# Optimization experiments

Hardware: AMD Instinct MI355X
Metric: run time of the kernel (lower is better)

The kernel has to match this reference:

```python
import jax, jax.numpy as jnp
import numpy as np

NEG_INF = -1e9

def apply_rope(x, positions, head_dim, theta):
    # x: [B, S, H, Dh]; positions: [S] int32
    half = head_dim // 2
    fraction = (2.0 / head_dim) * jnp.arange(half, dtype=jnp.float32)  # [Dh/2]
    timescale = theta ** fraction
    angle = positions.astype(jnp.float32)[:, None] / timescale  # [S, Dh/2]
    sin = jnp.sin(angle)[None, :, None, :]  # [1,S,1,Dh/2]
    cos = jnp.cos(angle)[None, :, None, :]
    x1, x2 = jnp.split(x, 2, axis=-1)
    out = jnp.concatenate([x1 * cos - x2 * sin, x2 * cos + x1 * sin], axis=-1)
    return out.astype(x.dtype)

def setup_inputs() -> dict:
    key = jax.random.key(0)
    B, S, D = 2, 2048, 2048
    Q, N, H = 16, 4, 128
    ks = jax.random.split(key, 5)
    scale = 1.0 / np.sqrt(D)
    return {
        "x": jax.random.normal(ks[0], (B, S, D), dtype=jnp.float32),
        "positions": jnp.arange(S, dtype=jnp.int32),
        "Wq": jax.random.normal(ks[1], (Q, D, H), dtype=jnp.float32) * scale,
        "Wk": jax.random.normal(ks[2], (N, D, H), dtype=jnp.float32) * scale,
        "Wv": jax.random.normal(ks[3], (N, D, H), dtype=jnp.float32) * scale,
        "Wo": jax.random.normal(ks[4], (Q, H, D), dtype=jnp.float32) * scale,
    }

def reference(x, positions, Wq, Wk, Wv, Wo):
    head_dim = Wq.shape[-1]
    theta = 10000.0
    head_repeats = Wq.shape[0] // Wk.shape[0]  # GQA repeat factor

    q_BSQH = jnp.einsum('BSD,QDH->BSQH', x, Wq)
    q_BSQH = apply_rope(q_BSQH, positions, head_dim, theta)
    k_BTNH = jnp.einsum('BSD,NDH->BSNH', x, Wk)
    k_BTNH = apply_rope(k_BTNH, positions, head_dim, theta)
    v_BTNH = jnp.einsum('BSD,NDH->BSNH', x, Wv)

    k_BTQH = jnp.repeat(k_BTNH, head_repeats, axis=2)
    v_BTQH = jnp.repeat(v_BTNH, head_repeats, axis=2)

    scores_BQST = jnp.einsum('BSQH,BTQH->BQST', q_BSQH, k_BTQH) / jnp.sqrt(
        jnp.asarray(head_dim, dtype=x.dtype))
    S = q_BSQH.shape[1]
    causal = jnp.tril(jnp.ones((1, 1, S, S), dtype=jnp.bool_))
    scores_BQST = jnp.where(causal, scores_BQST, NEG_INF)
    weights_BQST = jax.nn.softmax(scores_BQST, axis=-1)
    out_BSQH = jnp.einsum('BQST,BTQH->BSQH', weights_BQST, v_BTQH)
    o_BSD = jnp.einsum('BSQH,QHD->BSD', out_BSQH, Wo)
    return o_BSD
```

## Files before the change

kernel.cpp:

```cpp
#include <hip/hip_runtime.h>
#include <math.h>

#define BB 2
#define SS 2048
#define DD 2048
#define QH 16
#define NKV 4
#define HD 128
#define REP 4
#define NEG_INF_F (-1e9f)

typedef __bf16 bfrag __attribute__((ext_vector_type(8)));
typedef float  ffrag __attribute__((ext_vector_type(4)));

__device__ inline unsigned short f2bf(float f) {
    unsigned u = __builtin_bit_cast(unsigned, f);
    u += 0x7fff + ((u >> 16) & 1);
    return (unsigned short)(u >> 16);
}
__device__ inline float bf2f(unsigned short u) {
    unsigned v = (unsigned)u << 16;
    return __builtin_bit_cast(float, v);
}
__device__ inline bfrag ld_frag(const unsigned short* p) {
    uint4 u = *(const uint4*)p;
    return __builtin_bit_cast(bfrag, u);
}
__device__ inline void async16(const void* g, void* l) {
    __builtin_amdgcn_global_load_lds(
        (const __attribute__((address_space(1))) unsigned int*)g,
        (__attribute__((address_space(3))) unsigned int*)l, 16, 0, 0);
}
__device__ inline unsigned pkbf(float a, float b) {
    unsigned short ua = __builtin_bit_cast(unsigned short, (__bf16)a);
    unsigned short ub = __builtin_bit_cast(unsigned short, (__bf16)b);
    return (unsigned)ua | ((unsigned)ub << 16);
}

__global__ void cast_x_kernel(const float* __restrict__ x,
                              unsigned short* __restrict__ xb, int n)
{
    const int i = (blockIdx.x * blockDim.x + threadIdx.x) * 8;
    if (i >= n) return;
    float4 a = *(const float4*)(x + i);
    float4 b = *(const float4*)(x + i + 4);
    unsigned short o[8];
    o[0] = f2bf(a.x); o[1] = f2bf(a.y); o[2] = f2bf(a.z); o[3] = f2bf(a.w);
    o[4] = f2bf(b.x); o[5] = f2bf(b.y); o[6] = f2bf(b.z); o[7] = f2bf(b.w);
    *(uint4*)(xb + i) = *(uint4*)o;
}

__global__ __launch_bounds__(256) void tcast_kernel(
    const float* __restrict__ in, unsigned short* __restrict__ out,
    int R, int C)
{
    __shared__ float tile[32][33];
    const size_t bofs = (size_t)blockIdx.z * R * C;
    in  += bofs;
    out += bofs;
    const int c0 = blockIdx.x * 32, r0 = blockIdx.y * 32;
    const int tx = threadIdx.x & 31, ty = threadIdx.x >> 5;
    #pragma unroll
    for (int k = 0; k < 4; ++k)
        tile[ty + 8 * k][tx] = in[(size_t)(r0 + ty + 8 * k) * C + c0 + tx];
    __syncthreads();
    #pragma unroll
    for (int k = 0; k < 4; ++k)
        out[(size_t)(c0 + ty + 8 * k) * R + r0 + tx] =
            f2bf(tile[tx][ty + 8 * k]);
}

__global__ __launch_bounds__(256) void gemm_bt_kernel(
    const unsigned short* __restrict__ A,
    const unsigned short* __restrict__ Bt,
    unsigned short* __restrict__ q_out, unsigned short* __restrict__ k_out,
    unsigned short* __restrict__ vt_out, float* __restrict__ f_out,
    int mode)
{
    const int gy = gridDim.y;
    int f = blockIdx.x * gy + blockIdx.y;
    const int chunk = (gridDim.x * gy) >> 3;
    f = (f & 7) * chunk + (f >> 3);
    const int m0 = (f / gy) * 128;
    const int n0 = (f % gy) * 128;

    const int tid  = threadIdx.x;
    const int w    = tid >> 6, lane = tid & 63;
    const int l16  = lane & 15, quad = lane >> 4;
    const int wm = (w >> 1) * 64, wn = (w & 1) * 64;
    const int sl4 = l16 & 3;

    __shared__ unsigned short As[2][128 * 32];
    __shared__ unsigned short Bs[2][128 * 32];

    ffrag acc[4][4];
    #pragma unroll
    for (int mi = 0; mi < 4; ++mi)
        #pragma unroll
        for (int ni = 0; ni < 4; ++ni)
            acc[mi][ni] = (ffrag){0.f, 0.f, 0.f, 0.f};

    auto stage = [&](int b, int k0) {
        #pragma unroll
        for (int j = 0; j < 2; ++j) {
            const int i   = (j * 4 + w) * 64 + lane;
            const int row = i >> 2;
            const int sl  = (i & 3) ^ (row & 3);
            async16(&A [(size_t)(m0 + row) * 2048 + k0 + sl * 8],
                    (char*)&As[b][0] + i * 16);
            async16(&Bt[(size_t)(n0 + row) * 2048 + k0 + sl * 8],
                    (char*)&Bs[b][0] + i * 16);
        }
    };

    stage(0, 0);
    __syncthreads();
    int cur = 0;
    for (int k0 = 0; k0 < 2048; k0 += 32) {
        if (k0 + 32 < 2048) stage(cur ^ 1, k0 + 32);

        bfrag af[4], bfr[4];
        #pragma unroll
        for (int mi = 0; mi < 4; ++mi)
            af[mi] = ld_frag(
                &As[cur][(wm + mi * 16 + l16) * 32 + (quad ^ sl4) * 8]);
        #pragma unroll
        for (int ni = 0; ni < 4; ++ni)
            bfr[ni] = ld_frag(
                &Bs[cur][(wn + ni * 16 + l16) * 32 + (quad ^ sl4) * 8]);
        #pragma unroll
        for (int mi = 0; mi < 4; ++mi)
            #pragma unroll
            for (int ni = 0; ni < 4; ++ni)
                acc[mi][ni] = __builtin_amdgcn_mfma_f32_16x16x32_bf16(
                    af[mi], bfr[ni], acc[mi][ni], 0, 0, 0);

        __syncthreads();
        cur ^= 1;
    }

    if (mode == 0) {
        #pragma unroll
        for (int mi = 0; mi < 4; ++mi)
            #pragma unroll
            for (int ni = 0; ni < 4; ++ni) {
                const int col = n0 + wn + ni * 16 + l16;
                #pragma unroll
                for (int r = 0; r < 4; ++r) {
                    const int row = m0 + wm + mi * 16 + quad * 4 + r;
                    f_out[(size_t)row * 2048 + col] = acc[mi][ni][r];
                }
            }
    } else if (n0 < 2560) {
        unsigned short* dst;
        int colbase, stride;
        if (n0 < 2048)      { dst = q_out; colbase = n0;        stride = 2048; }
        else                { dst = k_out; colbase = n0 - 2048; stride = 512;  }
        #pragma unroll
        for (int mi = 0; mi < 4; ++mi)
            #pragma unroll
            for (int ni = 0; ni < 4; ++ni) {
                const int col = colbase + wn + ni * 16 + l16;
                #pragma unroll
                for (int r = 0; r < 4; ++r) {
                    const int row = m0 + wm + mi * 16 + quad * 4 + r;
                    dst[(size_t)row * stride + col] = f2bf(acc[mi][ni][r]);
                }
            }
    } else {
        const int c3 = n0 - 2560;
        #pragma unroll
        for (int mi = 0; mi < 4; ++mi)
            #pragma unroll
            for (int ni = 0; ni < 4; ++ni) {
                const int col = c3 + wn + ni * 16 + l16;
                const int nh = col >> 7, h = col & 127;
                const int row0 = m0 + wm + mi * 16 + quad * 4;
                const int b = row0 >> 11, s = row0 & 2047;
                unsigned short pk[4];
                #pragma unroll
                for (int r = 0; r < 4; ++r) pk[r] = f2bf(acc[mi][ni][r]);
                *(uint2*)&vt_out[(((size_t)b * NKV + nh) * HD + h) * SS + s] =
                    *(uint2*)pk;
            }
    }
}

__global__ void rope_kernel(unsigned short* __restrict__ q,
                            unsigned short* __restrict__ k,
                            const int* __restrict__ positions)
{
    const int qpairs = BB * SS * QH * 64;
    const int kpairs = BB * SS * NKV * 64;
    int idx = blockIdx.x * blockDim.x + threadIdx.x;
    unsigned short* base;
    int nh;
    if (idx < qpairs) { base = q; nh = QH; }
    else {
        idx -= qpairs;
        if (idx >= kpairs) return;
        base = k; nh = NKV;
    }
    const int hh   = idx & 63;
    const int rest = idx >> 6;
    const int head = rest % nh;
    const int bs   = rest / nh;
    const int s    = bs % SS;

    unsigned short* p = base + ((size_t)bs * nh + head) * HD;
    const float pos = (float)positions[s];
    const float inv_ts = powf(10000.0f, -(float)hh * (1.0f / 64.0f));
    const float angle = pos * inv_ts;
    const float sn = sinf(angle), cs = cosf(angle);
    const float sc_ = (nh == QH) ? 0.08838834764831845f : 1.0f;
    const float x1 = bf2f(p[hh]), x2 = bf2f(p[hh + 64]);
    p[hh]      = f2bf((x1 * cs - x2 * sn) * sc_);
    p[hh + 64] = f2bf((x2 * cs + x1 * sn) * sc_);
}

__global__ __launch_bounds__(256, 2) void attn_kernel(
    const unsigned short* __restrict__ qb,
    const unsigned short* __restrict__ kb,
    const unsigned short* __restrict__ vt,
    unsigned short* __restrict__ o)
{
    int f = blockIdx.y * 16 + blockIdx.x;
    f = (f & 7) * 64 + (f >> 3);
    const int bh = f >> 4;
    const int bx = f & 15;

    const int b  = bh / QH, qh = bh % QH;
    const int n  = qh / REP;

    const int tid  = threadIdx.x;
    const int w    = tid >> 6;
    const int lane = tid & 63;
    const int l16  = lane & 15;
    const int quad = lane >> 4;
    const int sw   = l16 & 7;

    __shared__ unsigned short Ks[2][2][64][64];
    __shared__ unsigned short Vs[2][128][64];
    __shared__ unsigned short Ps[4][16][72];

    const unsigned short* kbase = kb + (size_t)b * (SS * NKV * HD) + n * HD;
    const unsigned short* vbase = vt + ((size_t)b * NKV + n) * HD * SS;

    for (int ph = 0; ph < 2; ++ph) {
        const int tile = ph == 0 ? (31 - bx) : bx;
        const int s0 = tile * 64;
        const int rbase = s0 + w * 16 + quad * 4;
        const int thr   = w * 16 + l16;

        bfrag qf[4];
        {
            const unsigned short* qp =
                qb + ((size_t)(b * SS + s0 + w * 16 + l16) * QH + qh) * HD
                   + quad * 8;
            #pragma unroll
            for (int c = 0; c < 4; ++c) qf[c] = ld_frag(qp + c * 32);
        }
        ffrag oacc[8];
        #pragma unroll
        for (int t = 0; t < 8; ++t) oacc[t] = (ffrag){0.f, 0.f, 0.f, 0.f};
        float mr = -1e30f, lr = 0.0f;

        #pragma unroll
        for (int j = 0; j < 4; ++j) {
            const int s = j * 256 + tid;
            {   const int cc = s >> 9, t = (s >> 3) & 63;
                const int sl = (s & 7) ^ (t & 7);
                async16(kbase + (size_t)t * (NKV * HD) + cc * 64 + sl * 8,
                        (char*)&Ks[0][0][0][0] + s * 16);
            }
            {   const int h = s >> 3, sl = (s & 7) ^ (h & 7);
                async16(vbase + (size_t)h * SS + sl * 8,
                        (char*)&Vs[0][0][0] + s * 16);
            }
        }
        __syncthreads();

        int p = 0;
        for (int t0 = 0; t0 <= s0; t0 += 64, p ^= 1) {
            if (t0 + 64 <= s0) {
                const int tn = t0 + 64;
                #pragma unroll
                for (int j = 0; j < 4; ++j) {
                    const int s = j * 256 + tid;
                    {   const int cc = s >> 9, t = (s >> 3) & 63;
                        const int sl = (s & 7) ^ (t & 7);
                        async16(kbase + (size_t)(tn + t) * (NKV * HD)
                                      + cc * 64 + sl * 8,
                                (char*)&Ks[p ^ 1][0][0][0] + s * 16);
                    }
                    {   const int h = s >> 3, sl = (s & 7) ^ (h & 7);
                        async16(vbase + (size_t)h * SS + tn + sl * 8,
                                (char*)&Vs[p ^ 1][0][0] + s * 16);
                    }
                }
            }

            ffrag sc[4];
            #pragma unroll
            for (int t = 0; t < 4; ++t) sc[t] = (ffrag){0.f, 0.f, 0.f, 0.f};
            __builtin_amdgcn_s_setprio(1);
            #pragma unroll
            for (int c = 0; c < 4; ++c) {
                const int cc = c >> 1, cb = (c & 1) * 4;
                #pragma unroll
                for (int t = 0; t < 4; ++t) {
                    bfrag kfr = ld_frag(
                        &Ks[p][cc][t * 16 + l16][((cb + quad) ^ sw) * 8]);
                    sc[t] = __builtin_amdgcn_mfma_f32_16x16x32_bf16(
                        kfr, qf[c], sc[t], 0, 0, 0);
                }
            }
            __builtin_amdgcn_s_setprio(0);

            const bool diag = (t0 == s0);
            if (diag) {
                #pragma unroll
                for (int t = 0; t < 4; ++t) {
                    const int col0 = t * 16 + quad * 4;
                    #pragma unroll
                    for (int r = 0; r < 4; ++r)
                        if (col0 + r > thr) sc[t][r] = NEG_INF_F;
                }
            }

            float tmax;
            {
                float a0 = fmaxf(fmaxf(sc[0][0], sc[0][1]),
                                 fmaxf(sc[0][2], sc[0][3]));
                float a1 = fmaxf(fmaxf(sc[1][0], sc[1][1]),
                                 fmaxf(sc[1][2], sc[1][3]));
                float a2 = fmaxf(fmaxf(sc[2][0], sc[2][1]),
                                 fmaxf(sc[2][2], sc[2][3]));
                float a3 = fmaxf(fmaxf(sc[3][0], sc[3][1]),
                                 fmaxf(sc[3][2], sc[3][3]));
                tmax = fmaxf(fmaxf(a0, a1), fmaxf(a2, a3));
            }
            tmax = fmaxf(tmax, __shfl_xor(tmax, 16));
            tmax = fmaxf(tmax, __shfl_xor(tmax, 32));

            if (__any(tmax > mr + 8.0f)) {
                const float mnew  = fmaxf(mr, tmax);
                const float alpha = __expf(mr - mnew);
                lr *= alpha;
                mr = mnew;
                #pragma unroll
                for (int r = 0; r < 4; ++r) {
                    const float ar =
                        __shfl(alpha, (lane & 48) | (quad * 4 + r));
                    #pragma unroll
                    for (int t = 0; t < 8; ++t) oacc[t][r] *= ar;
                }
            }

            float ps = 0.f;
            #pragma unroll
            for (int t = 0; t < 4; ++t) {
                const float p0 = __expf(sc[t][0] - mr);
                const float p1 = __expf(sc[t][1] - mr);
                const float p2 = __expf(sc[t][2] - mr);
                const float p3 = __expf(sc[t][3] - mr);
                ps += (p0 + p1) + (p2 + p3);
                uint2 pk2;
                pk2.x = pkbf(p0, p1);
                pk2.y = pkbf(p2, p3);
                *(uint2*)&Ps[w][l16][t * 16 + quad * 4] = pk2;
            }
            ps += __shfl_xor(ps, 16);
            ps += __shfl_xor(ps, 32);
            lr += ps;

            __builtin_amdgcn_s_setprio(1);
            #pragma unroll
            for (int c = 0; c < 2; ++c) {
                bfrag pf = ld_frag(&Ps[w][l16][c * 32 + quad * 8]);
                #pragma unroll
                for (int t = 0; t < 8; ++t) {
                    bfrag vf = ld_frag(
                        &Vs[p][t * 16 + l16][((c * 4 + quad) ^ sw) * 8]);
                    oacc[t] = __builtin_amdgcn_mfma_f32_16x16x32_bf16(
                        pf, vf, oacc[t], 0, 0, 0);
                }
            }
            __builtin_amdgcn_s_setprio(0);

            __syncthreads();
        }

        #pragma unroll
        for (int r = 0; r < 4; ++r) {
            const float lrr  = __shfl(lr, (lane & 48) | (quad * 4 + r));
            const float invl = 1.0f / lrr;
            const int row = rbase + r;
            unsigned short* op = o + ((size_t)(b * SS + row) * QH + qh) * HD;
            #pragma unroll
            for (int t = 0; t < 8; ++t)
                op[t * 16 + l16] = f2bf(oacc[t][r] * invl);
        }
    }
}

extern "C" void kernel_launch(void* const* d_in, const int* in_sizes, int n_in,
                              void* d_out, int out_size, void* d_ws,
                              size_t ws_size, hipStream_t stream)
{
    const float* x         = (const float*)d_in[0];
    const int*   positions = (const int*)d_in[1];
    const float* Wq        = (const float*)d_in[2];
    const float* Wk        = (const float*)d_in[3];
    const float* Wv        = (const float*)d_in[4];
    const float* Wo        = (const float*)d_in[5];
    float* out = (float*)d_out;

    char* ws = (char*)d_ws;
    unsigned short* xb    = (unsigned short*)ws;
    unsigned short* Wqkvt = (unsigned short*)(ws + (16u << 20));
    unsigned short* Wot   = (unsigned short*)(ws + (28u << 20));
    unsigned short* qbf   = (unsigned short*)(ws + (36u << 20));
    unsigned short* kbf   = (unsigned short*)(ws + (52u << 20));
    unsigned short* vtb   = (unsigned short*)(ws + (56u << 20));
    unsigned short* opre  = xb;

    const int nx = BB * SS * DD;
    cast_x_kernel<<<nx / (8 * 256), 256, 0, stream>>>(x, xb, nx);

    tcast_kernel<<<dim3(4, 64, 16), 256, 0, stream>>>(Wq, Wqkvt, 2048, 128);
    tcast_kernel<<<dim3(4, 64, 4), 256, 0, stream>>>(
        Wk, Wqkvt + (size_t)16 * 128 * 2048, 2048, 128);
    tcast_kernel<<<dim3(4, 64, 4), 256, 0, stream>>>(
        Wv, Wqkvt + (size_t)20 * 128 * 2048, 2048, 128);
    tcast_kernel<<<dim3(64, 64, 1), 256, 0, stream>>>(Wo, Wot, 2048, 2048);

    gemm_bt_kernel<<<dim3(32, 24), 256, 0, stream>>>(
        xb, Wqkvt, qbf, kbf, vtb, nullptr, 1);

    const int pairs = BB * SS * (QH + NKV) * 64;
    rope_kernel<<<(pairs + 255) / 256, 256, 0, stream>>>(qbf, kbf, positions);

    dim3 g2(16, BB * QH);
    attn_kernel<<<g2, 256, 0, stream>>>(qbf, kbf, vtb, opre);

    gemm_bt_kernel<<<dim3(32, 16), 256, 0, stream>>>(
        opre, Wot, nullptr, nullptr, nullptr, out, 0);
}
```

Baseline: 361.0 us.

## Replace 128x128 GEMM with 256x256 tile, 4-stage async pipeline and MFMA priority

Both projection GEMMs now use a new kernel with 256x256 output tiles, 512 threads and a 4-deep shared-memory ring of async loads. It uses explicit vmcnt waits and barriers, and raises wave priority around the MFMA bursts. The aim is more reuse of each loaded tile and better hiding of global-load latency. The trade-off is far fewer blocks: 192 for the QKV GEMM and 128 for the output GEMM on a 256-CU device, so many CUs may sit idle. The old XCD-aware block remapping is also dropped.

```diff
diff --git a/kernel.cpp b/kernel.cpp
--- a/kernel.cpp
+++ b/kernel.cpp
@@ -70,85 +70,98 @@
             f2bf(tile[tx][ty + 8 * k]);
 }
 
-__global__ __launch_bounds__(256) void gemm_bt_kernel(
+__global__ __launch_bounds__(512, 2) void gemm256_kernel(
     const unsigned short* __restrict__ A,
     const unsigned short* __restrict__ Bt,
     unsigned short* __restrict__ q_out, unsigned short* __restrict__ k_out,
     unsigned short* __restrict__ vt_out, float* __restrict__ f_out,
     int mode)
 {
-    const int gy = gridDim.y;
-    int f = blockIdx.x * gy + blockIdx.y;
-    const int chunk = (gridDim.x * gy) >> 3;
-    f = (f & 7) * chunk + (f >> 3);
-    const int m0 = (f / gy) * 128;
-    const int n0 = (f % gy) * 128;
-
+    const int m0 = blockIdx.x * 256;
+    const int n0 = blockIdx.y * 256;
     const int tid  = threadIdx.x;
-    const int w    = tid >> 6, lane = tid & 63;
+    const int wid  = tid >> 6, lane = tid & 63;
     const int l16  = lane & 15, quad = lane >> 4;
-    const int wm = (w >> 1) * 64, wn = (w & 1) * 64;
-    const int sl4 = l16 & 3;
-
-    __shared__ unsigned short As[2][128 * 32];
-    __shared__ unsigned short Bs[2][128 * 32];
-
-    ffrag acc[4][4];
+    const int wr   = wid >> 2, wc = wid & 3;
+    const int rs   = quad ^ (l16 & 3);
+
+    __shared__ unsigned short As[4][256 * 32];
+    __shared__ unsigned short Bs[4][256 * 32];
+
+    ffrag acc[8][4];
     #pragma unroll
-    for (int mi = 0; mi < 4; ++mi)
-        #pragma unroll
-        for (int ni = 0; ni < 4; ++ni)
-            acc[mi][ni] = (ffrag){0.f, 0.f, 0.f, 0.f};
-
-    auto stage = [&](int b, int k0) {
+    for (int mf = 0; mf < 8; ++mf)
+        #pragma unroll
+        for (int nf = 0; nf < 4; ++nf)
+            acc[mf][nf] = (ffrag){0.f, 0.f, 0.f, 0.f};
+
+    auto stage = [&](int d, int t) {
+        const int k0 = t * 32;
         #pragma unroll
         for (int j = 0; j < 2; ++j) {
-            const int i   = (j * 4 + w) * 64 + lane;
+            const int i   = j * 512 + tid;
             const int row = i >> 2;
             const int sl  = (i & 3) ^ (row & 3);
             async16(&A [(size_t)(m0 + row) * 2048 + k0 + sl * 8],
-                    (char*)&As[b][0] + i * 16);
+                    (char*)&As[d][0] + i * 16);
             async16(&Bt[(size_t)(n0 + row) * 2048 + k0 + sl * 8],
-                    (char*)&Bs[b][0] + i * 16);
+                    (char*)&Bs[d][0] + i * 16);
         }
     };
 
-    stage(0, 0);
-    __syncthreads();
-    int cur = 0;
-    for (int k0 = 0; k0 < 2048; k0 += 32) {
-        if (k0 + 32 < 2048) stage(cur ^ 1, k0 + 32);
-
-        bfrag af[4], bfr[4];
-        #pragma unroll
-        for (int mi = 0; mi < 4; ++mi)
-            af[mi] = ld_frag(
-                &As[cur][(wm + mi * 16 + l16) * 32 + (quad ^ sl4) * 8]);
-        #pragma unroll
-        for (int ni = 0; ni < 4; ++ni)
-            bfr[ni] = ld_frag(
-                &Bs[cur][(wn + ni * 16 + l16) * 32 + (quad ^ sl4) * 8]);
-        #pragma unroll
-        for (int mi = 0; mi < 4; ++mi)
-            #pragma unroll
-            for (int ni = 0; ni < 4; ++ni)
-                acc[mi][ni] = __builtin_amdgcn_mfma_f32_16x16x32_bf16(
-                    af[mi], bfr[ni], acc[mi][ni], 0, 0, 0);
-
-        __syncthreads();
-        cur ^= 1;
+    stage(0, 0); stage(1, 1); stage(2, 2);
+    asm volatile("s_waitcnt vmcnt(8)" ::: "memory");
+    __builtin_amdgcn_s_barrier();
+    __builtin_amdgcn_sched_barrier(0);
+
+    for (int T = 0; T < 64; ++T) {
+        if (T + 3 < 64) stage((T + 3) & 3, T + 3);
+
+        const int d = T & 3;
+        const unsigned short* ab = &As[d][0];
+        const unsigned short* bb = &Bs[d][0];
+
+        bfrag bfr[4];
+        #pragma unroll
+        for (int nf = 0; nf < 4; ++nf)
+            bfr[nf] = ld_frag(&bb[(wc * 64 + nf * 16 + l16) * 32 + rs * 8]);
+
+        #pragma unroll
+        for (int q = 0; q < 4; ++q) {
+            bfrag a0 = ld_frag(
+                &ab[(wr * 128 + (q * 2) * 16 + l16) * 32 + rs * 8]);
+            bfrag a1 = ld_frag(
+                &ab[(wr * 128 + (q * 2 + 1) * 16 + l16) * 32 + rs * 8]);
+            __builtin_amdgcn_s_setprio(1);
+            #pragma unroll
+            for (int nf = 0; nf < 4; ++nf) {
+                acc[q * 2][nf] = __builtin_amdgcn_mfma_f32_16x16x32_bf16(
+                    a0, bfr[nf], acc[q * 2][nf], 0, 0, 0);
+                acc[q * 2 + 1][nf] = __builtin_amdgcn_mfma_f32_16x16x32_bf16(
+                    a1, bfr[nf], acc[q * 2 + 1][nf], 0, 0, 0);
+            }
+            __builtin_amdgcn_s_setprio(0);
+        }
+
+        if (T < 61)       asm volatile("s_waitcnt vmcnt(8)" ::: "memory");
+        else if (T == 61) asm volatile("s_waitcnt vmcnt(4)" ::: "memory");
+        else if (T == 62) asm volatile("s_waitcnt vmcnt(0)" ::: "memory");
+        if (T < 63) {
+            __builtin_amdgcn_s_barrier();
+            __builtin_amdgcn_sched_barrier(0);
+        }
     }
 
     if (mode == 0) {
         #pragma unroll
-        for (int mi = 0; mi < 4; ++mi)
-            #pragma unroll
-            for (int ni = 0; ni < 4; ++ni) {
-                const int col = n0 + wn + ni * 16 + l16;
+        for (int mf = 0; mf < 8; ++mf)
+            #pragma unroll
+            for (int nf = 0; nf < 4; ++nf) {
+                const int col = n0 + wc * 64 + nf * 16 + l16;
                 #pragma unroll
                 for (int r = 0; r < 4; ++r) {
-                    const int row = m0 + wm + mi * 16 + quad * 4 + r;
-                    f_out[(size_t)row * 2048 + col] = acc[mi][ni][r];
+                    const int row = m0 + wr * 128 + mf * 16 + quad * 4 + r;
+                    f_out[(size_t)row * 2048 + col] = acc[mf][nf][r];
                 }
             }
     } else if (n0 < 2560) {
@@ -157,29 +170,29 @@
         if (n0 < 2048)      { dst = q_out; colbase = n0;        stride = 2048; }
         else                { dst = k_out; colbase = n0 - 2048; stride = 512;  }
         #pragma unroll
-        for (int mi = 0; mi < 4; ++mi)
-            #pragma unroll
-            for (int ni = 0; ni < 4; ++ni) {
-                const int col = colbase + wn + ni * 16 + l16;
+        for (int mf = 0; mf < 8; ++mf)
+            #pragma unroll
+            for (int nf = 0; nf < 4; ++nf) {
+                const int col = colbase + wc * 64 + nf * 16 + l16;
                 #pragma unroll
                 for (int r = 0; r < 4; ++r) {
-                    const int row = m0 + wm + mi * 16 + quad * 4 + r;
-                    dst[(size_t)row * stride + col] = f2bf(acc[mi][ni][r]);
+                    const int row = m0 + wr * 128 + mf * 16 + quad * 4 + r;
+                    dst[(size_t)row * stride + col] = f2bf(acc[mf][nf][r]);
                 }
             }
     } else {
         const int c3 = n0 - 2560;
         #pragma unroll
-        for (int mi = 0; mi < 4; ++mi)
-            #pragma unroll
-            for (int ni = 0; ni < 4; ++ni) {
-                const int col = c3 + wn + ni * 16 + l16;
+        for (int mf = 0; mf < 8; ++mf)
+            #pragma unroll
+            for (int nf = 0; nf < 4; ++nf) {
+                const int col = c3 + wc * 64 + nf * 16 + l16;
                 const int nh = col >> 7, h = col & 127;
-                const int row0 = m0 + wm + mi * 16 + quad * 4;
+                const int row0 = m0 + wr * 128 + mf * 16 + quad * 4;
                 const int b = row0 >> 11, s = row0 & 2047;
                 unsigned short pk[4];
                 #pragma unroll
-                for (int r = 0; r < 4; ++r) pk[r] = f2bf(acc[mi][ni][r]);
+                for (int r = 0; r < 4; ++r) pk[r] = f2bf(acc[mf][nf][r]);
                 *(uint2*)&vt_out[(((size_t)b * NKV + nh) * HD + h) * SS + s] =
                     *(uint2*)pk;
             }
@@ -435,7 +448,7 @@
         Wv, Wqkvt + (size_t)20 * 128 * 2048, 2048, 128);
     tcast_kernel<<<dim3(64, 64, 1), 256, 0, stream>>>(Wo, Wot, 2048, 2048);
 
-    gemm_bt_kernel<<<dim3(32, 24), 256, 0, stream>>>(
+    gemm256_kernel<<<dim3(16, 12), 512, 0, stream>>>(
         xb, Wqkvt, qbf, kbf, vtb, nullptr, 1);
 
     const int pairs = BB * SS * (QH + NKV) * 64;
@@ -444,6 +457,6 @@
     dim3 g2(16, BB * QH);
     attn_kernel<<<g2, 256, 0, stream>>>(qbf, kbf, vtb, opre);
 
-    gemm_bt_kernel<<<dim3(32, 16), 256, 0, stream>>>(
+    gemm256_kernel<<<dim3(16, 8), 512, 0, stream>>>(
         opre, Wot, nullptr, nullptr, nullptr, out, 0);
 }
```

Measured after the change: 385.1 us. 6.7% more time.
